# Optimization experiments

Measured on AMD Instinct MI355X. Metric: run time of the kernel, lower is better.

Reference implementation:

```python
import jax, jax.numpy as jnp
import numpy as np

B, S, H = 4, 4096, 1024
E, K, DE, DS = 8, 2, 128, 512  # n_routed_experts, top_k, routed hidden, shared hidden


def setup_inputs() -> dict:
    key = jax.random.key(0)
    ks = jax.random.split(key, 10)
    sc = 0.02
    return {
        "x": jax.random.normal(ks[0], (B, S, H), dtype=jnp.float32),
        "Wg": jax.random.normal(ks[1], (E, H), dtype=jnp.float32) * sc,
        "W1": jax.random.normal(ks[2], (E, DE, H), dtype=jnp.float32) * sc,
        "b1": jnp.zeros((E, DE), dtype=jnp.float32),
        "W2": jax.random.normal(ks[3], (E, H, DE), dtype=jnp.float32) * sc,
        "b2": jnp.zeros((E, H), dtype=jnp.float32),
        "Ws1": jax.random.normal(ks[4], (DS, H), dtype=jnp.float32) * sc,
        "bs1": jnp.zeros((DS,), dtype=jnp.float32),
        "Ws2": jax.random.normal(ks[5], (H, DS), dtype=jnp.float32) * sc,
        "bs2": jnp.zeros((H,), dtype=jnp.float32),
    }


def reference(x, Wg, W1, b1, W2, b2, Ws1, bs1, Ws2, bs2):
    # FFNMoE forward, eval mode (dropout = identity, aux loss inactive).
    xf = x.reshape(-1, H)  # [T, H]
    # --- MOEGate: softmax scoring + top-k + normalized weights ---
    logits = xf @ Wg.T                         # [T, E]
    scores = jax.nn.softmax(logits, axis=-1)
    topk_w, topk_idx = jax.lax.top_k(scores, K)  # [T, K]
    topk_w = topk_w / (jnp.sum(topk_w, axis=-1, keepdims=True) + 1e-20)
    # Dense per-(token, expert) combine weight (topk indices are distinct).
    w = jnp.sum(jax.nn.one_hot(topk_idx, E, dtype=xf.dtype) * topk_w[..., None], axis=1)  # [T, E]
    # --- Routed experts: fc1 -> relu -> fc2, weighted scatter-combine ---
    h1 = jax.nn.relu(jnp.einsum('th,efh->tef', xf, W1) + b1)       # [T, E, DE]
    y = jnp.einsum('tef,ehf,te->th', h1, W2, w) + w @ b2           # [T, H]
    # --- Shared expert ---
    sh = jax.nn.relu(xf @ Ws1.T + bs1) @ Ws2.T + bs2               # [T, H]
    return (y + sh).reshape(x.shape)
```

## Files before the change

kernel.cpp:

```cpp
#include <hip/hip_runtime.h>
#include <cstdint>

#define TTOK 16384
#define HD   1024
#define NE   8
#define NDE  128
#define NDS  512
#define NC1  1536
#define KC2  1536
#define NPAIR 28
#define MAXT  160
#define PREPB 3080
#define GATEB 1024
#define NH    768

typedef float  f32x4  __attribute__((ext_vector_type(4)));
typedef __bf16 bf16x8 __attribute__((ext_vector_type(8)));

__device__ __forceinline__ unsigned short f2bf(float f) {
  unsigned int u = __float_as_uint(f);
  u += 0x7fffu + ((u >> 16) & 1u);
  return (unsigned short)(u >> 16);
}

__device__ __forceinline__ void gl2lds16(const void* gp, void* lp) {
  void* g0 = const_cast<void*>(gp);
  __builtin_amdgcn_global_load_lds((__attribute__((address_space(1))) void*)g0,
                                   (__attribute__((address_space(3))) void*)lp,
                                   16, 0, 0);
}

__global__ __launch_bounds__(256) void prep_gate(
    const float* __restrict__ x, const float* __restrict__ Wg,
    const float* __restrict__ W1, const float* __restrict__ Ws1,
    const float* __restrict__ W2, const float* __restrict__ Ws2,
    const float* __restrict__ b1, const float* __restrict__ bs1,
    unsigned short* __restrict__ W1cat, unsigned short* __restrict__ W2cat,
    float* __restrict__ bias1, unsigned short* __restrict__ xbf,
    float2* __restrict__ wpair, int* __restrict__ pid) {
  if (blockIdx.x < PREPB) {
    const int total = NC1 * HD + HD * KC2 + NC1;
    for (int idx = blockIdx.x * 256 + threadIdx.x; idx < total; idx += PREPB * 256) {
      if (idx < NC1 * HD) {
        int r = idx >> 10, k = idx & 1023;
        float v = (r < 1024) ? W1[idx] : Ws1[(size_t)(r - 1024) * HD + k];
        W1cat[idx] = f2bf(v);
      } else if (idx < NC1 * HD + HD * KC2) {
        int i2 = idx - NC1 * HD;
        int h = i2 / KC2;
        int j = i2 - h * KC2;
        float v = (j < 1024) ? W2[(size_t)((j >> 7) * HD + h) * NDE + (j & 127)]
                             : Ws2[(size_t)h * NDS + (j - 1024)];
        W2cat[i2] = f2bf(v);
      } else {
        int r = idx - (NC1 * HD + HD * KC2);
        bias1[r] = (r < 1024) ? b1[r] : bs1[r - 1024];
      }
    }
    return;
  }
  __shared__ float part[16 * 8 * 64];
  __shared__ float lgs[128];

  const int tid  = threadIdx.x;
  const int lane = tid & 63;
  const int wv   = tid >> 6;
  const int g    = blockIdx.x - PREPB;
  const int tokb = g * 16 + wv * 4;

  const float* xr = x + (size_t)tokb * HD + lane * 16;
  float4 xv[4][4];
#pragma unroll
  for (int t = 0; t < 4; ++t)
#pragma unroll
    for (int c = 0; c < 4; ++c)
      xv[t][c] = ((const float4*)(xr + (size_t)t * HD))[c];

#pragma unroll
  for (int t = 0; t < 4; ++t) {
    unsigned short* xo = xbf + (size_t)(tokb + t) * HD + lane * 16;
    union { unsigned short us[8]; uint4 v; } pk;
    pk.us[0] = f2bf(xv[t][0].x); pk.us[1] = f2bf(xv[t][0].y);
    pk.us[2] = f2bf(xv[t][0].z); pk.us[3] = f2bf(xv[t][0].w);
    pk.us[4] = f2bf(xv[t][1].x); pk.us[5] = f2bf(xv[t][1].y);
    pk.us[6] = f2bf(xv[t][1].z); pk.us[7] = f2bf(xv[t][1].w);
    ((uint4*)xo)[0] = pk.v;
    pk.us[0] = f2bf(xv[t][2].x); pk.us[1] = f2bf(xv[t][2].y);
    pk.us[2] = f2bf(xv[t][2].z); pk.us[3] = f2bf(xv[t][2].w);
    pk.us[4] = f2bf(xv[t][3].x); pk.us[5] = f2bf(xv[t][3].y);
    pk.us[6] = f2bf(xv[t][3].z); pk.us[7] = f2bf(xv[t][3].w);
    ((uint4*)xo)[1] = pk.v;
  }

  float p[4][8];
#pragma unroll
  for (int t = 0; t < 4; ++t)
#pragma unroll
    for (int e = 0; e < 8; ++e) p[t][e] = 0.f;
#pragma unroll
  for (int e = 0; e < 8; ++e) {
    const float4* wr = (const float4*)(Wg + (size_t)e * HD + lane * 16);
    float4 w0 = wr[0], w1 = wr[1], w2 = wr[2], w3 = wr[3];
#pragma unroll
    for (int t = 0; t < 4; ++t) {
      p[t][e] = w0.x * xv[t][0].x + w0.y * xv[t][0].y + w0.z * xv[t][0].z + w0.w * xv[t][0].w +
                w1.x * xv[t][1].x + w1.y * xv[t][1].y + w1.z * xv[t][1].z + w1.w * xv[t][1].w +
                w2.x * xv[t][2].x + w2.y * xv[t][2].y + w2.z * xv[t][2].z + w2.w * xv[t][2].w +
                w3.x * xv[t][3].x + w3.y * xv[t][3].y + w3.z * xv[t][3].z + w3.w * xv[t][3].w;
    }
  }
#pragma unroll
  for (int t = 0; t < 4; ++t)
#pragma unroll
    for (int e = 0; e < 8; ++e) {
      int j = (wv * 4 + t) * 8 + e;
      part[j * 64 + ((lane + 4 * j) & 63)] = p[t][e];
    }
  __syncthreads();

  if (tid < 128) {
    float s = 0.f;
#pragma unroll
    for (int m = 0; m < 16; ++m) {
      int kk = (4 * m + 4 * tid) & 63;
      float4 v = *(const float4*)&part[tid * 64 + kk];
      s += v.x + v.y + v.z + v.w;
    }
    lgs[tid] = s;
  }
  __syncthreads();

  if (tid < 16) {
    float lg[8];
#pragma unroll
    for (int e = 0; e < 8; ++e) lg[e] = lgs[tid * 8 + e];
    int i1 = 0; float m1 = lg[0];
#pragma unroll
    for (int e = 1; e < 8; ++e) { if (lg[e] > m1) { m1 = lg[e]; i1 = e; } }
    int i2 = -1; float m2 = -3.4e38f;
#pragma unroll
    for (int e = 0; e < 8; ++e) { if (e != i1 && lg[e] > m2) { m2 = lg[e]; i2 = e; } }
    float Z = 0.f;
#pragma unroll
    for (int e = 0; e < 8; ++e) Z += expf(lg[e] - m1);
    float s1 = 1.f / Z;
    float s2 = expf(m2 - m1) / Z;
    float dn = s1 + s2 + 1e-20f;
    float w1 = s1 / dn, w2 = s2 / dn;
    int ef, es; float wf, wsx;
    if (i1 < i2) { ef = i1; es = i2; wf = w1; wsx = w2; }
    else         { ef = i2; es = i1; wf = w2; wsx = w1; }
    int pq = ef * 7 - (ef * (ef - 1)) / 2 + (es - ef - 1);
    int t = g * 16 + tid;
    wpair[t] = make_float2(wf, wsx);
    pid[t] = pq;
  }
}

__global__ __launch_bounds__(256) void route_scan(const int* __restrict__ pid,
                                                  int* __restrict__ perm,
                                                  int4* __restrict__ tiletab,
                                                  int* __restrict__ ntct) {
  __shared__ int hist[256 * 29];
  __shared__ int totals[NPAIR];
  __shared__ int spre[256];
  const int p   = blockIdx.x;
  const int tid = threadIdx.x;
#pragma unroll
  for (int q = 0; q < 29; ++q) hist[tid * 29 + q] = 0;
  __syncthreads();
  for (int k = 0; k < 64; ++k) {
    int q = pid[tid + (k << 8)];
    hist[tid * 29 + q]++;
  }
  __syncthreads();
  if (tid < NPAIR) {
    int s = 0;
    for (int i = 0; i < 256; ++i) s += hist[i * 29 + tid];
    totals[tid] = s;
  }
  __syncthreads();
  const int mycnt = hist[tid * 29 + p];
  spre[tid] = mycnt;
  __syncthreads();
  for (int d = 1; d < 256; d <<= 1) {
    int add = (tid >= d) ? spre[tid - d] : 0;
    __syncthreads();
    spre[tid] += add;
    __syncthreads();
  }
  int estart = 0, tstart = 0;
  for (int q = 0; q < p; ++q) { estart += totals[q]; tstart += (totals[q] + 127) >> 7; }
  const int cp = totals[p];
  const int nt = (cp + 127) >> 7;
  if (p == NPAIR - 1 && tid == 0) ntct[0] = tstart + nt;
  for (int k = tid; k < nt; k += 256) {
    int4 e;
    e.x = p;
    e.y = estart + (k << 7);
    e.z = min(128, cp - (k << 7));
    e.w = (tstart + k) << 7;
    tiletab[tstart + k] = e;
  }
  int wr = estart + spre[tid] - mycnt;
  for (int k = 0; k < 64; ++k) {
    int t = tid + (k << 8);
    if (pid[t] == p) perm[wr++] = t;
  }
}

__global__ __launch_bounds__(256) void moe_fc1(const unsigned short* __restrict__ xbf,
                                               const unsigned short* __restrict__ W1cat,
                                               const int* __restrict__ perm,
                                               const float2* __restrict__ wpair,
                                               const float* __restrict__ bias1,
                                               const int4* __restrict__ tiletab,
                                               const int* __restrict__ ntct,
                                               unsigned short* __restrict__ Hbuf) {
  const int L   = blockIdx.x;
  const int xcd = L & 7;
  const int s   = L >> 3;
  const int mg  = s / 6;
  const int nn  = s - mg * 6;
  const int mt  = xcd + (mg << 3);
  if (mt >= ntct[0]) return;
  const int4 tt = tiletab[mt];
  const int eoff = tt.y, valid = tt.z, hbase = tt.w;
  int ef = 0, rem = tt.x;
  while (rem >= 7 - ef) { rem -= 7 - ef; ef++; }
  const int es = ef + 1 + rem;
  const int brow = (nn == 0) ? ef * 128 : (nn == 1) ? es * 128 : 1024 + ((nn - 2) << 7);

  __shared__ __align__(16) unsigned short As[128 * 64];
  __shared__ __align__(16) unsigned short Bs[128 * 64];

  const int tid  = threadIdx.x;
  const int lane = tid & 63;
  const int wv   = tid >> 6;
  const int wm   = wv >> 1;
  const int wn   = wv & 1;
  const int r16  = lane & 15;
  const int quad = lane >> 4;

  const unsigned short* gA[4];
  const unsigned short* gB[4];
  unsigned short* lA[4];
  unsigned short* lB[4];
#pragma unroll
  for (int i = 0; i < 4; ++i) {
    int idx = i * 256 + tid;
    int row = idx >> 3;
    int cc  = idx & 7;
    int kc  = cc ^ (row & 7);
    int tok = perm[eoff + min(row, valid - 1)];
    gA[i] = xbf + (size_t)tok * HD + kc * 8;
    gB[i] = W1cat + (size_t)(brow + row) * HD + kc * 8;
    lA[i] = As + idx * 8;
    lB[i] = Bs + idx * 8;
  }

  int aoff[4], boff[4];
#pragma unroll
  for (int i = 0; i < 4; ++i) {
    int ra = wm * 64 + i * 16 + r16;
    aoff[i] = ra * 64 + ((quad ^ (ra & 7)) << 3);
    int rb = wn * 64 + i * 16 + r16;
    boff[i] = rb * 64 + ((quad ^ (rb & 7)) << 3);
  }

  f32x4 acc[4][4];
#pragma unroll
  for (int i = 0; i < 4; ++i)
#pragma unroll
    for (int j = 0; j < 4; ++j) acc[i][j] = (f32x4){0.f, 0.f, 0.f, 0.f};

  for (int kt = 0; kt < 16; ++kt) {
    const int ko = kt << 6;
#pragma unroll
    for (int i = 0; i < 4; ++i) gl2lds16(gA[i] + ko, lA[i]);
#pragma unroll
    for (int i = 0; i < 4; ++i) gl2lds16(gB[i] + ko, lB[i]);
    __syncthreads();
#pragma unroll
    for (int g = 0; g < 2; ++g) {
      const int gx = g << 5;
      bf16x8 av[4], bv[4];
#pragma unroll
      for (int i = 0; i < 4; ++i) av[i] = *(const bf16x8*)(As + (aoff[i] ^ gx));
#pragma unroll
      for (int j = 0; j < 4; ++j) bv[j] = *(const bf16x8*)(Bs + (boff[j] ^ gx));
#pragma unroll
      for (int i = 0; i < 4; ++i)
#pragma unroll
        for (int j = 0; j < 4; ++j)
          acc[i][j] = __builtin_amdgcn_mfma_f32_16x16x32_bf16(av[i], bv[j], acc[i][j], 0, 0, 0);
    }
    __syncthreads();
  }

  float* wl = (float*)As;
  if (tid < 128) {
    int tok = perm[eoff + min(tid, valid - 1)];
    float sc = 1.0f;
    if (nn == 0) sc = wpair[tok].x;
    else if (nn == 1) sc = wpair[tok].y;
    wl[tid] = sc;
  }
  __syncthreads();
#pragma unroll
  for (int j = 0; j < 4; ++j) {
    const int cin = wn * 64 + j * 16 + r16;
    const float bz = bias1[brow + cin];
#pragma unroll
    for (int i = 0; i < 4; ++i) {
#pragma unroll
      for (int r = 0; r < 4; ++r) {
        const int lrow = wm * 64 + i * 16 + quad * 4 + r;
        float v = fmaxf(acc[i][j][r] + bz, 0.f) * wl[lrow];
        Hbuf[(size_t)(hbase + lrow) * NH + nn * 128 + cin] = f2bf(v);
      }
    }
  }
}

__global__ __launch_bounds__(256) void moe_fc2(const unsigned short* __restrict__ Hbuf,
                                               const unsigned short* __restrict__ W2cat,
                                               const int* __restrict__ perm,
                                               const float2* __restrict__ wpair,
                                               const float* __restrict__ b2,
                                               const float* __restrict__ bs2,
                                               const int4* __restrict__ tiletab,
                                               const int* __restrict__ ntct,
                                               float* __restrict__ out) {
  const int L   = blockIdx.x;
  const int xcd = L & 7;
  const int s   = L >> 3;
  const int mg  = s >> 3;
  const int nn  = s & 7;
  const int mt  = xcd + (mg << 3);
  if (mt >= ntct[0]) return;
  const int4 tt = tiletab[mt];
  const int eoff = tt.y, valid = tt.z, hbase = tt.w;
  int ef = 0, rem = tt.x;
  while (rem >= 7 - ef) { rem -= 7 - ef; ef++; }
  const int es = ef + 1 + rem;
  const int tileN = nn << 7;

  __shared__ __align__(16) unsigned short As[128 * 64];
  __shared__ __align__(16) unsigned short Bs[128 * 64];

  const int tid  = threadIdx.x;
  const int lane = tid & 63;
  const int wv   = tid >> 6;
  const int wm   = wv >> 1;
  const int wn   = wv & 1;
  const int r16  = lane & 15;
  const int quad = lane >> 4;

  const unsigned short* gA[4];
  const unsigned short* gB[4];
  unsigned short* lA[4];
  unsigned short* lB[4];
#pragma unroll
  for (int i = 0; i < 4; ++i) {
    int idx = i * 256 + tid;
    int row = idx >> 3;
    int cc  = idx & 7;
    int kc  = cc ^ (row & 7);
    gA[i] = Hbuf + (size_t)(hbase + row) * NH + kc * 8;
    gB[i] = W2cat + (size_t)(tileN + row) * KC2 + kc * 8;
    lA[i] = As + idx * 8;
    lB[i] = Bs + idx * 8;
  }

  int aoff[4], boff[4];
#pragma unroll
  for (int i = 0; i < 4; ++i) {
    int ra = wm * 64 + i * 16 + r16;
    aoff[i] = ra * 64 + ((quad ^ (ra & 7)) << 3);
    int rb = wn * 64 + i * 16 + r16;
    boff[i] = rb * 64 + ((quad ^ (rb & 7)) << 3);
  }

  f32x4 acc[4][4];
#pragma unroll
  for (int i = 0; i < 4; ++i)
#pragma unroll
    for (int j = 0; j < 4; ++j) acc[i][j] = (f32x4){0.f, 0.f, 0.f, 0.f};

  for (int kt = 0; kt < 12; ++kt) {
    const int koA = kt << 6;
    const int koB = (kt < 2) ? ef * 128 + (kt << 6)
                 : (kt < 4) ? es * 128 + ((kt - 2) << 6)
                            : 1024 + ((kt - 4) << 6);
#pragma unroll
    for (int i = 0; i < 4; ++i) gl2lds16(gA[i] + koA, lA[i]);
#pragma unroll
    for (int i = 0; i < 4; ++i) gl2lds16(gB[i] + koB, lB[i]);
    __syncthreads();
#pragma unroll
    for (int g = 0; g < 2; ++g) {
      const int gx = g << 5;
      bf16x8 av[4], bv[4];
#pragma unroll
      for (int i = 0; i < 4; ++i) av[i] = *(const bf16x8*)(As + (aoff[i] ^ gx));
#pragma unroll
      for (int j = 0; j < 4; ++j) bv[j] = *(const bf16x8*)(Bs + (boff[j] ^ gx));
#pragma unroll
      for (int i = 0; i < 4; ++i)
#pragma unroll
        for (int j = 0; j < 4; ++j)
          acc[i][j] = __builtin_amdgcn_mfma_f32_16x16x32_bf16(av[i], bv[j], acc[i][j], 0, 0, 0);
    }
    __syncthreads();
  }

  float2* wl2 = (float2*)As;
  int* tokl   = (int*)Bs;
  if (tid < 128) {
    int tokc = perm[eoff + min(tid, valid - 1)];
    tokl[tid] = (tid < valid) ? tokc : -1;
    wl2[tid] = wpair[tokc];
  }
  __syncthreads();
  float bsc[4], b2a[4], b2b[4];
#pragma unroll
  for (int j = 0; j < 4; ++j) {
    const int col = tileN + wn * 64 + j * 16 + r16;
    bsc[j] = bs2[col];
    b2a[j] = b2[(size_t)ef * HD + col];
    b2b[j] = b2[(size_t)es * HD + col];
  }
#pragma unroll
  for (int i = 0; i < 4; ++i) {
#pragma unroll
    for (int r = 0; r < 4; ++r) {
      const int lrow = wm * 64 + i * 16 + quad * 4 + r;
      const int tok = tokl[lrow];
      if (tok < 0) continue;
      const float2 w = wl2[lrow];
#pragma unroll
      for (int j = 0; j < 4; ++j) {
        const int col = tileN + wn * 64 + j * 16 + r16;
        out[(size_t)tok * HD + col] = acc[i][j][r] + bsc[j] + w.x * b2a[j] + w.y * b2b[j];
      }
    }
  }
}

extern "C" void kernel_launch(void* const* d_in, const int* in_sizes, int n_in,
                              void* d_out, int out_size, void* d_ws, size_t ws_size,
                              hipStream_t stream) {
  const float* x   = (const float*)d_in[0];
  const float* Wg  = (const float*)d_in[1];
  const float* W1  = (const float*)d_in[2];
  const float* b1  = (const float*)d_in[3];
  const float* W2  = (const float*)d_in[4];
  const float* b2  = (const float*)d_in[5];
  const float* Ws1 = (const float*)d_in[6];
  const float* bs1 = (const float*)d_in[7];
  const float* Ws2 = (const float*)d_in[8];
  const float* bs2 = (const float*)d_in[9];

  char* ws = (char*)d_ws;
  size_t off = 0;
  unsigned short* xbf   = (unsigned short*)(ws + off); off += (size_t)TTOK * HD * 2;
  unsigned short* Hbuf  = (unsigned short*)(ws + off); off += (size_t)MAXT * 128 * NH * 2;
  unsigned short* W1cat = (unsigned short*)(ws + off); off += (size_t)NC1 * HD * 2;
  unsigned short* W2cat = (unsigned short*)(ws + off); off += (size_t)HD * KC2 * 2;
  float* bias1          = (float*)(ws + off);          off += (size_t)NC1 * 4;
  float2* wpair         = (float2*)(ws + off);         off += (size_t)TTOK * 8;
  int* pid              = (int*)(ws + off);            off += (size_t)TTOK * 4;
  int* perm             = (int*)(ws + off);            off += (size_t)TTOK * 4;
  int4* tiletab         = (int4*)(ws + off);           off += (size_t)MAXT * 16;
  int* ntct             = (int*)(ws + off);            off += 16;

  prep_gate<<<PREPB + GATEB, 256, 0, stream>>>(x, Wg, W1, Ws1, W2, Ws2, b1, bs1,
                                               W1cat, W2cat, bias1, xbf, wpair, pid);
  route_scan<<<NPAIR, 256, 0, stream>>>(pid, perm, tiletab, ntct);
  moe_fc1<<<8 * 20 * 6, 256, 0, stream>>>(xbf, W1cat, perm, wpair, bias1, tiletab, ntct, Hbuf);
  moe_fc2<<<8 * 20 * 8, 256, 0, stream>>>(Hbuf, W2cat, perm, wpair, b2, bs2, tiletab, ntct,
                                          (float*)d_out);
}
```

Measured before the change: 250.1 us.

## Use 256x256 tiles with double-buffered 8-wave pipelined MFMA GEMMs for MoE

```diff
diff --git a/kernel.cpp b/kernel.cpp
--- a/kernel.cpp
+++ b/kernel.cpp
@@ -9,7 +9,7 @@
 #define NC1  1536
 #define KC2  1536
 #define NPAIR 28
-#define MAXT  160
+#define MAXT  96
 #define PREPB 3080
 #define GATEB 1024
 #define NH    768
@@ -29,6 +29,60 @@
                                    (__attribute__((address_space(3))) void*)lp,
                                    16, 0, 0);
 }
+
+__device__ __forceinline__ void barx() {
+  asm volatile("" ::: "memory");
+  __builtin_amdgcn_s_barrier();
+  asm volatile("" ::: "memory");
+}
+
+template<int Q>
+__device__ __forceinline__ void phase_reads(const unsigned short* Ab, const unsigned short* Bb,
+                                            int bs, int a0, int b0,
+                                            bf16x8 (&av)[4][2], bf16x8 (&bv)[2][2]) {
+  constexpr int MH = Q >> 1, NHF = Q & 1;
+  if constexpr (NHF == 0) {
+#pragma unroll
+    for (int m = 0; m < 4; ++m) {
+      const int ao = a0 + (MH * 4 + m) * 1024;
+      av[m][0] = *(const bf16x8*)(Ab + bs + ao);
+      av[m][1] = *(const bf16x8*)(Ab + bs + (ao ^ 32));
+    }
+  }
+#pragma unroll
+  for (int n = 0; n < 2; ++n) {
+    const int bo = b0 + (NHF * 2 + n) * 1024;
+    bv[n][0] = *(const bf16x8*)(Bb + bs + bo);
+    bv[n][1] = *(const bf16x8*)(Bb + bs + (bo ^ 32));
+  }
+}
+
+template<int Q>
+__device__ __forceinline__ void phase_mfma(bf16x8 (&av)[4][2], bf16x8 (&bv)[2][2],
+                                           f32x4 (&acc)[8][4]) {
+  constexpr int MH = Q >> 1, NHF = Q & 1;
+  __builtin_amdgcn_s_setprio(1);
+#pragma unroll
+  for (int ks = 0; ks < 2; ++ks)
+#pragma unroll
+    for (int m = 0; m < 4; ++m)
+#pragma unroll
+      for (int n = 0; n < 2; ++n)
+        acc[MH * 4 + m][NHF * 2 + n] = __builtin_amdgcn_mfma_f32_16x16x32_bf16(
+            av[m][ks], bv[n][ks], acc[MH * 4 + m][NHF * 2 + n], 0, 0, 0);
+  __builtin_amdgcn_s_setprio(0);
+}
+
+#define PH(Q, BH, STG, VMW) do {                                    \
+    phase_reads<Q>(AsB, BsB, (BH) * 16384, a0, b0, av, bv);         \
+    STG;                                                            \
+    VMW;                                                            \
+    barx();                                                         \
+    asm volatile("s_waitcnt lgkmcnt(0)" ::: "memory");              \
+    __builtin_amdgcn_sched_barrier(0);                              \
+    phase_mfma<Q>(av, bv, acc);                                     \
+    barx();                                                         \
+  } while (0)
 
 __global__ __launch_bounds__(256) void prep_gate(
     const float* __restrict__ x, const float* __restrict__ Wg,
@@ -190,16 +244,16 @@
     __syncthreads();
   }
   int estart = 0, tstart = 0;
-  for (int q = 0; q < p; ++q) { estart += totals[q]; tstart += (totals[q] + 127) >> 7; }
+  for (int q = 0; q < p; ++q) { estart += totals[q]; tstart += (totals[q] + 255) >> 8; }
   const int cp = totals[p];
-  const int nt = (cp + 127) >> 7;
+  const int nt = (cp + 255) >> 8;
   if (p == NPAIR - 1 && tid == 0) ntct[0] = tstart + nt;
   for (int k = tid; k < nt; k += 256) {
     int4 e;
     e.x = p;
-    e.y = estart + (k << 7);
-    e.z = min(128, cp - (k << 7));
-    e.w = (tstart + k) << 7;
+    e.y = estart + (k << 8);
+    e.z = min(256, cp - (k << 8));
+    e.w = (tstart + k) << 8;
     tiletab[tstart + k] = e;
   }
   int wr = estart + spre[tid] - mycnt;
@@ -209,19 +263,16 @@
   }
 }
 
-__global__ __launch_bounds__(256) void moe_fc1(const unsigned short* __restrict__ xbf,
-                                               const unsigned short* __restrict__ W1cat,
-                                               const int* __restrict__ perm,
-                                               const float2* __restrict__ wpair,
-                                               const float* __restrict__ bias1,
-                                               const int4* __restrict__ tiletab,
-                                               const int* __restrict__ ntct,
-                                               unsigned short* __restrict__ Hbuf) {
+__global__ __launch_bounds__(512, 2) void moe_fc1(
+    const unsigned short* __restrict__ xbf, const unsigned short* __restrict__ W1cat,
+    const int* __restrict__ perm, const float2* __restrict__ wpair,
+    const float* __restrict__ bias1, const int4* __restrict__ tiletab,
+    const int* __restrict__ ntct, unsigned short* __restrict__ Hbuf) {
   const int L   = blockIdx.x;
   const int xcd = L & 7;
   const int s   = L >> 3;
-  const int mg  = s / 6;
-  const int nn  = s - mg * 6;
+  const int mg  = s / 3;
+  const int nn  = s - mg * 3;
   const int mt  = xcd + (mg << 3);
   if (mt >= ntct[0]) return;
   const int4 tt = tiletab[mt];
@@ -229,114 +280,138 @@
   int ef = 0, rem = tt.x;
   while (rem >= 7 - ef) { rem -= 7 - ef; ef++; }
   const int es = ef + 1 + rem;
-  const int brow = (nn == 0) ? ef * 128 : (nn == 1) ? es * 128 : 1024 + ((nn - 2) << 7);
-
-  __shared__ __align__(16) unsigned short As[128 * 64];
-  __shared__ __align__(16) unsigned short Bs[128 * 64];
+
+  __shared__ __align__(16) unsigned short As[2 * 16384];
+  __shared__ __align__(16) unsigned short Bs[2 * 16384];
 
   const int tid  = threadIdx.x;
   const int lane = tid & 63;
   const int wv   = tid >> 6;
-  const int wm   = wv >> 1;
-  const int wn   = wv & 1;
+  const int wm   = wv >> 2;
+  const int wn   = wv & 3;
   const int r16  = lane & 15;
   const int quad = lane >> 4;
 
-  const unsigned short* gA[4];
-  const unsigned short* gB[4];
-  unsigned short* lA[4];
-  unsigned short* lB[4];
-#pragma unroll
-  for (int i = 0; i < 4; ++i) {
-    int idx = i * 256 + tid;
-    int row = idx >> 3;
-    int cc  = idx & 7;
-    int kc  = cc ^ (row & 7);
-    int tok = perm[eoff + min(row, valid - 1)];
-    gA[i] = xbf + (size_t)tok * HD + kc * 8;
-    gB[i] = W1cat + (size_t)(brow + row) * HD + kc * 8;
-    lA[i] = As + idx * 8;
-    lB[i] = Bs + idx * 8;
-  }
-
-  int aoff[4], boff[4];
-#pragma unroll
-  for (int i = 0; i < 4; ++i) {
-    int ra = wm * 64 + i * 16 + r16;
-    aoff[i] = ra * 64 + ((quad ^ (ra & 7)) << 3);
-    int rb = wn * 64 + i * 16 + r16;
-    boff[i] = rb * 64 + ((quad ^ (rb & 7)) << 3);
-  }
-
-  f32x4 acc[4][4];
-#pragma unroll
-  for (int i = 0; i < 4; ++i)
+  const unsigned short* gAp[2][2];
+  const unsigned short* gBp[2][2];
+  int lAo[2][2], lBo[2][2];
+#pragma unroll
+  for (int h = 0; h < 2; ++h)
+#pragma unroll
+    for (int jj = 0; jj < 2; ++jj) {
+      const int id = jj * 512 + tid;
+      const int rp = id >> 3, cc = id & 7;
+      const int rowA = h * 64 + ((rp & 64) << 1) + (rp & 63);
+      const int tok  = perm[eoff + min(rowA, valid - 1)];
+      gAp[h][jj] = xbf + (size_t)tok * HD + ((cc ^ (rowA & 7)) << 3);
+      lAo[h][jj] = rowA * 64 + cc * 8;
+      const int rowB = h * 128 + rp;
+      const int brow = (nn == 0) ? (((h == 0) ? ef : es) * 128 + rp)
+                                 : 1024 + (nn - 1) * 256 + rowB;
+      gBp[h][jj] = W1cat + (size_t)brow * HD + ((cc ^ (rowB & 7)) << 3);
+      lBo[h][jj] = rowB * 64 + cc * 8;
+    }
+
+  unsigned short* AsB = As;
+  unsigned short* BsB = Bs;
+
+  const int swz = (quad ^ (r16 & 7)) << 3;
+  const int a0 = (wm * 128 + r16) * 64 + swz;
+  const int b0 = (wn * 64 + r16) * 64 + swz;
+
+  f32x4 acc[8][4];
+#pragma unroll
+  for (int i = 0; i < 8; ++i)
 #pragma unroll
     for (int j = 0; j < 4; ++j) acc[i][j] = (f32x4){0.f, 0.f, 0.f, 0.f};
-
-  for (int kt = 0; kt < 16; ++kt) {
-    const int ko = kt << 6;
-#pragma unroll
-    for (int i = 0; i < 4; ++i) gl2lds16(gA[i] + ko, lA[i]);
-#pragma unroll
-    for (int i = 0; i < 4; ++i) gl2lds16(gB[i] + ko, lB[i]);
-    __syncthreads();
-#pragma unroll
-    for (int g = 0; g < 2; ++g) {
-      const int gx = g << 5;
-      bf16x8 av[4], bv[4];
-#pragma unroll
-      for (int i = 0; i < 4; ++i) av[i] = *(const bf16x8*)(As + (aoff[i] ^ gx));
-#pragma unroll
-      for (int j = 0; j < 4; ++j) bv[j] = *(const bf16x8*)(Bs + (boff[j] ^ gx));
-#pragma unroll
-      for (int i = 0; i < 4; ++i)
-#pragma unroll
-        for (int j = 0; j < 4; ++j)
-          acc[i][j] = __builtin_amdgcn_mfma_f32_16x16x32_bf16(av[i], bv[j], acc[i][j], 0, 0, 0);
-    }
-    __syncthreads();
-  }
-
-  float* wl = (float*)As;
-  if (tid < 128) {
-    int tok = perm[eoff + min(tid, valid - 1)];
-    float sc = 1.0f;
-    if (nn == 0) sc = wpair[tok].x;
-    else if (nn == 1) sc = wpair[tok].y;
-    wl[tid] = sc;
-  }
-  __syncthreads();
-#pragma unroll
-  for (int j = 0; j < 4; ++j) {
-    const int cin = wn * 64 + j * 16 + r16;
-    const float bz = bias1[brow + cin];
-#pragma unroll
-    for (int i = 0; i < 4; ++i) {
-#pragma unroll
-      for (int r = 0; r < 4; ++r) {
-        const int lrow = wm * 64 + i * 16 + quad * 4 + r;
-        float v = fmaxf(acc[i][j][r] + bz, 0.f) * wl[lrow];
-        Hbuf[(size_t)(hbase + lrow) * NH + nn * 128 + cin] = f2bf(v);
+  bf16x8 av[4][2], bv[2][2];
+
+#define STG_A1K(t, h) do { const int b_ = (((t) & 1) << 14); const int o_ = ((t) << 6); \
+    gl2lds16(gAp[h][0] + o_, AsB + b_ + lAo[h][0]);                                     \
+    gl2lds16(gAp[h][1] + o_, AsB + b_ + lAo[h][1]); } while (0)
+#define STG_B1K(t, h) do { const int b_ = (((t) & 1) << 14); const int o_ = ((t) << 6); \
+    gl2lds16(gBp[h][0] + o_, BsB + b_ + lBo[h][0]);                                     \
+    gl2lds16(gBp[h][1] + o_, BsB + b_ + lBo[h][1]); } while (0)
+
+  STG_A1K(0, 0); STG_A1K(0, 1);
+  STG_B1K(0, 0); STG_B1K(0, 1);
+  STG_A1K(1, 0); STG_A1K(1, 1);
+  asm volatile("s_waitcnt vmcnt(4)" ::: "memory");
+  barx();
+
+#define FC1_ITER(it, LASTF) do {                                                   \
+    const int O1 = 2 * (it) + 1, E2 = 2 * (it) + 2, O2 = 2 * (it) + 3;             \
+    PH(0, 0, STG_B1K(O1, 0), (void)0);                                             \
+    PH(1, 0, STG_B1K(O1, 1), (void)0);                                             \
+    PH(2, 0, { if (!(LASTF)) STG_A1K(E2, 0); }, (void)0);                          \
+    PH(3, 0, { if (!(LASTF)) STG_A1K(E2, 1); },                                    \
+        { if (LASTF) asm volatile("s_waitcnt vmcnt(0)" ::: "memory");              \
+          else       asm volatile("s_waitcnt vmcnt(4)" ::: "memory"); });          \
+    PH(0, 1, { if (!(LASTF)) STG_B1K(E2, 0); }, (void)0);                          \
+    PH(1, 1, { if (!(LASTF)) STG_B1K(E2, 1); }, (void)0);                          \
+    PH(2, 1, { if (!(LASTF)) STG_A1K(O2, 0); }, (void)0);                          \
+    PH(3, 1, { if (!(LASTF)) STG_A1K(O2, 1); },                                    \
+        { if (LASTF) asm volatile("s_waitcnt vmcnt(0)" ::: "memory");              \
+          else       asm volatile("s_waitcnt vmcnt(4)" ::: "memory"); });          \
+  } while (0)
+
+#pragma unroll 1
+  for (int it = 0; it < 7; ++it) FC1_ITER(it, 0);
+  FC1_ITER(7, 1);
+
+  __syncthreads();
+  float2* wl = (float2*)As;
+  if (tid < 256) {
+    const int tokc = perm[eoff + min(tid, valid - 1)];
+    wl[tid] = wpair[tokc];
+  }
+  __syncthreads();
+  float bz[4];
+  const int colb = wn * 64 + r16;
+#pragma unroll
+  for (int n2 = 0; n2 < 4; ++n2) {
+    const int col = colb + n2 * 16;
+    const int bidx = (nn == 0) ? ((col < 128) ? ef * 128 + col : es * 128 + (col - 128))
+                               : 1024 + (nn - 1) * 256 + col;
+    bz[n2] = bias1[bidx];
+  }
+#pragma unroll
+  for (int m2 = 0; m2 < 8; ++m2) {
+#pragma unroll
+    for (int r = 0; r < 4; ++r) {
+      const int lrow = wm * 128 + m2 * 16 + quad * 4 + r;
+      const float2 w = wl[lrow];
+      const float sc = (nn == 0) ? ((wn < 2) ? w.x : w.y) : 1.0f;
+      unsigned short* hp = Hbuf + (size_t)(hbase + lrow) * NH + nn * 256 + colb;
+#pragma unroll
+      for (int n2 = 0; n2 < 4; ++n2) {
+        const float v = fmaxf(acc[m2][n2][r] + bz[n2], 0.f) * sc;
+        hp[n2 * 16] = f2bf(v);
       }
     }
   }
-}
-
-__global__ __launch_bounds__(256) void moe_fc2(const unsigned short* __restrict__ Hbuf,
-                                               const unsigned short* __restrict__ W2cat,
-                                               const int* __restrict__ perm,
-                                               const float2* __restrict__ wpair,
-                                               const float* __restrict__ b2,
-                                               const float* __restrict__ bs2,
-                                               const int4* __restrict__ tiletab,
-                                               const int* __restrict__ ntct,
-                                               float* __restrict__ out) {
+#undef FC1_ITER
+#undef STG_A1K
+#undef STG_B1K
+}
+
+__device__ __forceinline__ int koB2(int t, int ef, int es) {
+  return (t < 2) ? ef * 128 + (t << 6)
+       : (t < 4) ? es * 128 + ((t - 2) << 6)
+                 : 1024 + ((t - 4) << 6);
+}
+
+__global__ __launch_bounds__(512, 2) void moe_fc2(
+    const unsigned short* __restrict__ Hbuf, const unsigned short* __restrict__ W2cat,
+    const int* __restrict__ perm, const float2* __restrict__ wpair,
+    const float* __restrict__ b2, const float* __restrict__ bs2,
+    const int4* __restrict__ tiletab, const int* __restrict__ ntct,
+    float* __restrict__ out) {
   const int L   = blockIdx.x;
   const int xcd = L & 7;
   const int s   = L >> 3;
-  const int mg  = s >> 3;
-  const int nn  = s & 7;
+  const int mg  = s >> 2;
+  const int nn  = s & 3;
   const int mt  = xcd + (mg << 3);
   if (mt >= ntct[0]) return;
   const int4 tt = tiletab[mt];
@@ -344,108 +419,118 @@
   int ef = 0, rem = tt.x;
   while (rem >= 7 - ef) { rem -= 7 - ef; ef++; }
   const int es = ef + 1 + rem;
-  const int tileN = nn << 7;
-
-  __shared__ __align__(16) unsigned short As[128 * 64];
-  __shared__ __align__(16) unsigned short Bs[128 * 64];
+  const int tileN = nn << 8;
+
+  __shared__ __align__(16) unsigned short As[2 * 16384];
+  __shared__ __align__(16) unsigned short Bs[2 * 16384];
 
   const int tid  = threadIdx.x;
   const int lane = tid & 63;
   const int wv   = tid >> 6;
-  const int wm   = wv >> 1;
-  const int wn   = wv & 1;
+  const int wm   = wv >> 2;
+  const int wn   = wv & 3;
   const int r16  = lane & 15;
   const int quad = lane >> 4;
 
-  const unsigned short* gA[4];
-  const unsigned short* gB[4];
-  unsigned short* lA[4];
-  unsigned short* lB[4];
-#pragma unroll
-  for (int i = 0; i < 4; ++i) {
-    int idx = i * 256 + tid;
-    int row = idx >> 3;
-    int cc  = idx & 7;
-    int kc  = cc ^ (row & 7);
-    gA[i] = Hbuf + (size_t)(hbase + row) * NH + kc * 8;
-    gB[i] = W2cat + (size_t)(tileN + row) * KC2 + kc * 8;
-    lA[i] = As + idx * 8;
-    lB[i] = Bs + idx * 8;
-  }
-
-  int aoff[4], boff[4];
-#pragma unroll
-  for (int i = 0; i < 4; ++i) {
-    int ra = wm * 64 + i * 16 + r16;
-    aoff[i] = ra * 64 + ((quad ^ (ra & 7)) << 3);
-    int rb = wn * 64 + i * 16 + r16;
-    boff[i] = rb * 64 + ((quad ^ (rb & 7)) << 3);
-  }
-
-  f32x4 acc[4][4];
-#pragma unroll
-  for (int i = 0; i < 4; ++i)
+  const unsigned short* gAp[2][2];
+  const unsigned short* gBp[2][2];
+  int lAo[2][2], lBo[2][2];
+#pragma unroll
+  for (int h = 0; h < 2; ++h)
+#pragma unroll
+    for (int jj = 0; jj < 2; ++jj) {
+      const int id = jj * 512 + tid;
+      const int rp = id >> 3, cc = id & 7;
+      const int rowA = h * 64 + ((rp & 64) << 1) + (rp & 63);
+      gAp[h][jj] = Hbuf + (size_t)(hbase + rowA) * NH + ((cc ^ (rowA & 7)) << 3);
+      lAo[h][jj] = rowA * 64 + cc * 8;
+      const int rowB = h * 128 + rp;
+      gBp[h][jj] = W2cat + (size_t)(tileN + rowB) * KC2 + ((cc ^ (rowB & 7)) << 3);
+      lBo[h][jj] = rowB * 64 + cc * 8;
+    }
+
+  unsigned short* AsB = As;
+  unsigned short* BsB = Bs;
+
+  const int swz = (quad ^ (r16 & 7)) << 3;
+  const int a0 = (wm * 128 + r16) * 64 + swz;
+  const int b0 = (wn * 64 + r16) * 64 + swz;
+
+  f32x4 acc[8][4];
+#pragma unroll
+  for (int i = 0; i < 8; ++i)
 #pragma unroll
     for (int j = 0; j < 4; ++j) acc[i][j] = (f32x4){0.f, 0.f, 0.f, 0.f};
-
-  for (int kt = 0; kt < 12; ++kt) {
-    const int koA = kt << 6;
-    const int koB = (kt < 2) ? ef * 128 + (kt << 6)
-                 : (kt < 4) ? es * 128 + ((kt - 2) << 6)
-                            : 1024 + ((kt - 4) << 6);
-#pragma unroll
-    for (int i = 0; i < 4; ++i) gl2lds16(gA[i] + koA, lA[i]);
-#pragma unroll
-    for (int i = 0; i < 4; ++i) gl2lds16(gB[i] + koB, lB[i]);
-    __syncthreads();
-#pragma unroll
-    for (int g = 0; g < 2; ++g) {
-      const int gx = g << 5;
-      bf16x8 av[4], bv[4];
-#pragma unroll
-      for (int i = 0; i < 4; ++i) av[i] = *(const bf16x8*)(As + (aoff[i] ^ gx));
-#pragma unroll
-      for (int j = 0; j < 4; ++j) bv[j] = *(const bf16x8*)(Bs + (boff[j] ^ gx));
-#pragma unroll
-      for (int i = 0; i < 4; ++i)
-#pragma unroll
-        for (int j = 0; j < 4; ++j)
-          acc[i][j] = __builtin_amdgcn_mfma_f32_16x16x32_bf16(av[i], bv[j], acc[i][j], 0, 0, 0);
-    }
-    __syncthreads();
-  }
-
+  bf16x8 av[4][2], bv[2][2];
+
+#define STG_A2K(t, h) do { const int b_ = (((t) & 1) << 14); const int o_ = ((t) << 6); \
+    gl2lds16(gAp[h][0] + o_, AsB + b_ + lAo[h][0]);                                     \
+    gl2lds16(gAp[h][1] + o_, AsB + b_ + lAo[h][1]); } while (0)
+#define STG_B2K(t, h) do { const int b_ = (((t) & 1) << 14); const int o_ = koB2((t), ef, es); \
+    gl2lds16(gBp[h][0] + o_, BsB + b_ + lBo[h][0]);                                     \
+    gl2lds16(gBp[h][1] + o_, BsB + b_ + lBo[h][1]); } while (0)
+
+  STG_A2K(0, 0); STG_A2K(0, 1);
+  STG_B2K(0, 0); STG_B2K(0, 1);
+  STG_A2K(1, 0); STG_A2K(1, 1);
+  asm volatile("s_waitcnt vmcnt(4)" ::: "memory");
+  barx();
+
+#define FC2_ITER(it, LASTF) do {                                                   \
+    const int O1 = 2 * (it) + 1, E2 = 2 * (it) + 2, O2 = 2 * (it) + 3;             \
+    PH(0, 0, STG_B2K(O1, 0), (void)0);                                             \
+    PH(1, 0, STG_B2K(O1, 1), (void)0);                                             \
+    PH(2, 0, { if (!(LASTF)) STG_A2K(E2, 0); }, (void)0);                          \
+    PH(3, 0, { if (!(LASTF)) STG_A2K(E2, 1); },                                    \
+        { if (LASTF) asm volatile("s_waitcnt vmcnt(0)" ::: "memory");              \
+          else       asm volatile("s_waitcnt vmcnt(4)" ::: "memory"); });          \
+    PH(0, 1, { if (!(LASTF)) STG_B2K(E2, 0); }, (void)0);                          \
+    PH(1, 1, { if (!(LASTF)) STG_B2K(E2, 1); }, (void)0);                          \
+    PH(2, 1, { if (!(LASTF)) STG_A2K(O2, 0); }, (void)0);                          \
+    PH(3, 1, { if (!(LASTF)) STG_A2K(O2, 1); },                                    \
+        { if (LASTF) asm volatile("s_waitcnt vmcnt(0)" ::: "memory");              \
+          else       asm volatile("s_waitcnt vmcnt(4)" ::: "memory"); });          \
+  } while (0)
+
+#pragma unroll 1
+  for (int it = 0; it < 5; ++it) FC2_ITER(it, 0);
+  FC2_ITER(5, 1);
+
+  __syncthreads();
   float2* wl2 = (float2*)As;
   int* tokl   = (int*)Bs;
-  if (tid < 128) {
-    int tokc = perm[eoff + min(tid, valid - 1)];
+  if (tid < 256) {
+    const int tokc = perm[eoff + min(tid, valid - 1)];
     tokl[tid] = (tid < valid) ? tokc : -1;
     wl2[tid] = wpair[tokc];
   }
   __syncthreads();
   float bsc[4], b2a[4], b2b[4];
-#pragma unroll
-  for (int j = 0; j < 4; ++j) {
-    const int col = tileN + wn * 64 + j * 16 + r16;
-    bsc[j] = bs2[col];
-    b2a[j] = b2[(size_t)ef * HD + col];
-    b2b[j] = b2[(size_t)es * HD + col];
-  }
-#pragma unroll
-  for (int i = 0; i < 4; ++i) {
+  const int colb = tileN + wn * 64 + r16;
+#pragma unroll
+  for (int n2 = 0; n2 < 4; ++n2) {
+    const int col = colb + n2 * 16;
+    bsc[n2] = bs2[col];
+    b2a[n2] = b2[(size_t)ef * HD + col];
+    b2b[n2] = b2[(size_t)es * HD + col];
+  }
+#pragma unroll
+  for (int m2 = 0; m2 < 8; ++m2) {
 #pragma unroll
     for (int r = 0; r < 4; ++r) {
-      const int lrow = wm * 64 + i * 16 + quad * 4 + r;
+      const int lrow = wm * 128 + m2 * 16 + quad * 4 + r;
       const int tok = tokl[lrow];
       if (tok < 0) continue;
       const float2 w = wl2[lrow];
-#pragma unroll
-      for (int j = 0; j < 4; ++j) {
-        const int col = tileN + wn * 64 + j * 16 + r16;
-        out[(size_t)tok * HD + col] = acc[i][j][r] + bsc[j] + w.x * b2a[j] + w.y * b2b[j];
-      }
-    }
-  }
+      float* op = out + (size_t)tok * HD + colb;
+#pragma unroll
+      for (int n2 = 0; n2 < 4; ++n2)
+        op[n2 * 16] = acc[m2][n2][r] + bsc[n2] + w.x * b2a[n2] + w.y * b2b[n2];
+    }
+  }
+#undef FC2_ITER
+#undef STG_A2K
+#undef STG_B2K
 }
 
 extern "C" void kernel_launch(void* const* d_in, const int* in_sizes, int n_in,
@@ -465,7 +550,7 @@
   char* ws = (char*)d_ws;
   size_t off = 0;
   unsigned short* xbf   = (unsigned short*)(ws + off); off += (size_t)TTOK * HD * 2;
-  unsigned short* Hbuf  = (unsigned short*)(ws + off); off += (size_t)MAXT * 128 * NH * 2;
+  unsigned short* Hbuf  = (unsigned short*)(ws + off); off += (size_t)MAXT * 256 * NH * 2;
   unsigned short* W1cat = (unsigned short*)(ws + off); off += (size_t)NC1 * HD * 2;
   unsigned short* W2cat = (unsigned short*)(ws + off); off += (size_t)HD * KC2 * 2;
   float* bias1          = (float*)(ws + off);          off += (size_t)NC1 * 4;
@@ -478,7 +563,7 @@
   prep_gate<<<PREPB + GATEB, 256, 0, stream>>>(x, Wg, W1, Ws1, W2, Ws2, b1, bs1,
                                                W1cat, W2cat, bias1, xbf, wpair, pid);
   route_scan<<<NPAIR, 256, 0, stream>>>(pid, perm, tiletab, ntct);
-  moe_fc1<<<8 * 20 * 6, 256, 0, stream>>>(xbf, W1cat, perm, wpair, bias1, tiletab, ntct, Hbuf);
-  moe_fc2<<<8 * 20 * 8, 256, 0, stream>>>(Hbuf, W2cat, perm, wpair, b2, bs2, tiletab, ntct,
+  moe_fc1<<<8 * 12 * 3, 512, 0, stream>>>(xbf, W1cat, perm, wpair, bias1, tiletab, ntct, Hbuf);
+  moe_fc2<<<8 * 12 * 4, 512, 0, stream>>>(Hbuf, W2cat, perm, wpair, b2, bs2, tiletab, ntct,
                                           (float*)d_out);
 }
```

After: 294.7 us. +17.8%, slower.

## Double-buffer LDS tiles in both MoE GEMM kernels with async prefetch

Applied to the files above, without the earlier changes.

```diff
diff --git a/kernel.cpp b/kernel.cpp
--- a/kernel.cpp
+++ b/kernel.cpp
@@ -29,6 +29,14 @@
                                    (__attribute__((address_space(3))) void*)lp,
                                    16, 0, 0);
 }
+
+__device__ __forceinline__ void barx() {
+  asm volatile("" ::: "memory");
+  __builtin_amdgcn_s_barrier();
+  asm volatile("" ::: "memory");
+}
+#define VM8  asm volatile("s_waitcnt vmcnt(8)" ::: "memory")
+#define VM0  asm volatile("s_waitcnt vmcnt(0)" ::: "memory")
 
 __global__ __launch_bounds__(256) void prep_gate(
     const float* __restrict__ x, const float* __restrict__ Wg,
@@ -231,8 +239,8 @@
   const int es = ef + 1 + rem;
   const int brow = (nn == 0) ? ef * 128 : (nn == 1) ? es * 128 : 1024 + ((nn - 2) << 7);
 
-  __shared__ __align__(16) unsigned short As[128 * 64];
-  __shared__ __align__(16) unsigned short Bs[128 * 64];
+  __shared__ __align__(16) unsigned short As[2 * 128 * 64];
+  __shared__ __align__(16) unsigned short Bs[2 * 128 * 64];
 
   const int tid  = threadIdx.x;
   const int lane = tid & 63;
@@ -274,30 +282,44 @@
 #pragma unroll
     for (int j = 0; j < 4; ++j) acc[i][j] = (f32x4){0.f, 0.f, 0.f, 0.f};
 
-  for (int kt = 0; kt < 16; ++kt) {
-    const int ko = kt << 6;
-#pragma unroll
-    for (int i = 0; i < 4; ++i) gl2lds16(gA[i] + ko, lA[i]);
-#pragma unroll
-    for (int i = 0; i < 4; ++i) gl2lds16(gB[i] + ko, lB[i]);
-    __syncthreads();
-#pragma unroll
-    for (int g = 0; g < 2; ++g) {
-      const int gx = g << 5;
-      bf16x8 av[4], bv[4];
-#pragma unroll
-      for (int i = 0; i < 4; ++i) av[i] = *(const bf16x8*)(As + (aoff[i] ^ gx));
-#pragma unroll
-      for (int j = 0; j < 4; ++j) bv[j] = *(const bf16x8*)(Bs + (boff[j] ^ gx));
-#pragma unroll
-      for (int i = 0; i < 4; ++i)
-#pragma unroll
-        for (int j = 0; j < 4; ++j)
-          acc[i][j] = __builtin_amdgcn_mfma_f32_16x16x32_bf16(av[i], bv[j], acc[i][j], 0, 0, 0);
-    }
-    __syncthreads();
-  }
-
+#define STAGE1(kt, b) do { const int ko_ = (kt) << 6; const int lo_ = (b) * 8192;        \
+    _Pragma("unroll")                                                                    \
+    for (int i_ = 0; i_ < 4; ++i_) gl2lds16(gA[i_] + ko_, lA[i_] + lo_);                 \
+    _Pragma("unroll")                                                                    \
+    for (int i_ = 0; i_ < 4; ++i_) gl2lds16(gB[i_] + ko_, lB[i_] + lo_); } while (0)
+
+#define COMP1(b) do { const int lo_ = (b) * 8192;                                        \
+    _Pragma("unroll")                                                                    \
+    for (int g_ = 0; g_ < 2; ++g_) {                                                     \
+      const int gx_ = g_ << 5;                                                           \
+      bf16x8 av_[4], bv_[4];                                                             \
+      _Pragma("unroll")                                                                  \
+      for (int i_ = 0; i_ < 4; ++i_) av_[i_] = *(const bf16x8*)(As + lo_ + (aoff[i_] ^ gx_)); \
+      _Pragma("unroll")                                                                  \
+      for (int j_ = 0; j_ < 4; ++j_) bv_[j_] = *(const bf16x8*)(Bs + lo_ + (boff[j_] ^ gx_)); \
+      _Pragma("unroll")                                                                  \
+      for (int i_ = 0; i_ < 4; ++i_)                                                     \
+        _Pragma("unroll")                                                                \
+        for (int j_ = 0; j_ < 4; ++j_)                                                   \
+          acc[i_][j_] = __builtin_amdgcn_mfma_f32_16x16x32_bf16(av_[i_], bv_[j_], acc[i_][j_], 0, 0, 0); \
+    } } while (0)
+
+  STAGE1(0, 0);
+#pragma unroll 1
+  for (int kt = 0; kt < 16; kt += 2) {
+    if (kt + 1 < 16) { STAGE1(kt + 1, 1); VM8; } else { VM0; }
+    barx();
+    COMP1(0);
+    barx();
+    if (kt + 2 < 16) { STAGE1(kt + 2, 0); VM8; } else { VM0; }
+    barx();
+    COMP1(1);
+    barx();
+  }
+#undef STAGE1
+#undef COMP1
+
+  __syncthreads();
   float* wl = (float*)As;
   if (tid < 128) {
     int tok = perm[eoff + min(tid, valid - 1)];
@@ -346,8 +368,8 @@
   const int es = ef + 1 + rem;
   const int tileN = nn << 7;
 
-  __shared__ __align__(16) unsigned short As[128 * 64];
-  __shared__ __align__(16) unsigned short Bs[128 * 64];
+  __shared__ __align__(16) unsigned short As[2 * 128 * 64];
+  __shared__ __align__(16) unsigned short Bs[2 * 128 * 64];
 
   const int tid  = threadIdx.x;
   const int lane = tid & 63;
@@ -388,33 +410,49 @@
 #pragma unroll
     for (int j = 0; j < 4; ++j) acc[i][j] = (f32x4){0.f, 0.f, 0.f, 0.f};
 
-  for (int kt = 0; kt < 12; ++kt) {
-    const int koA = kt << 6;
-    const int koB = (kt < 2) ? ef * 128 + (kt << 6)
-                 : (kt < 4) ? es * 128 + ((kt - 2) << 6)
-                            : 1024 + ((kt - 4) << 6);
-#pragma unroll
-    for (int i = 0; i < 4; ++i) gl2lds16(gA[i] + koA, lA[i]);
-#pragma unroll
-    for (int i = 0; i < 4; ++i) gl2lds16(gB[i] + koB, lB[i]);
-    __syncthreads();
-#pragma unroll
-    for (int g = 0; g < 2; ++g) {
-      const int gx = g << 5;
-      bf16x8 av[4], bv[4];
-#pragma unroll
-      for (int i = 0; i < 4; ++i) av[i] = *(const bf16x8*)(As + (aoff[i] ^ gx));
-#pragma unroll
-      for (int j = 0; j < 4; ++j) bv[j] = *(const bf16x8*)(Bs + (boff[j] ^ gx));
-#pragma unroll
-      for (int i = 0; i < 4; ++i)
-#pragma unroll
-        for (int j = 0; j < 4; ++j)
-          acc[i][j] = __builtin_amdgcn_mfma_f32_16x16x32_bf16(av[i], bv[j], acc[i][j], 0, 0, 0);
-    }
-    __syncthreads();
-  }
-
+#define KOB2(kt) ((kt) < 2 ? ef * 128 + ((kt) << 6)                       \
+                : (kt) < 4 ? es * 128 + (((kt) - 2) << 6)                 \
+                           : 1024 + (((kt) - 4) << 6))
+#define STAGE2(kt, b) do { const int koA_ = (kt) << 6; const int koB_ = KOB2(kt);        \
+    const int lo_ = (b) * 8192;                                                          \
+    _Pragma("unroll")                                                                    \
+    for (int i_ = 0; i_ < 4; ++i_) gl2lds16(gA[i_] + koA_, lA[i_] + lo_);                \
+    _Pragma("unroll")                                                                    \
+    for (int i_ = 0; i_ < 4; ++i_) gl2lds16(gB[i_] + koB_, lB[i_] + lo_); } while (0)
+
+#define COMP2(b) do { const int lo_ = (b) * 8192;                                        \
+    _Pragma("unroll")                                                                    \
+    for (int g_ = 0; g_ < 2; ++g_) {                                                     \
+      const int gx_ = g_ << 5;                                                           \
+      bf16x8 av_[4], bv_[4];                                                             \
+      _Pragma("unroll")                                                                  \
+      for (int i_ = 0; i_ < 4; ++i_) av_[i_] = *(const bf16x8*)(As + lo_ + (aoff[i_] ^ gx_)); \
+      _Pragma("unroll")                                                                  \
+      for (int j_ = 0; j_ < 4; ++j_) bv_[j_] = *(const bf16x8*)(Bs + lo_ + (boff[j_] ^ gx_)); \
+      _Pragma("unroll")                                                                  \
+      for (int i_ = 0; i_ < 4; ++i_)                                                     \
+        _Pragma("unroll")                                                                \
+        for (int j_ = 0; j_ < 4; ++j_)                                                   \
+          acc[i_][j_] = __builtin_amdgcn_mfma_f32_16x16x32_bf16(av_[i_], bv_[j_], acc[i_][j_], 0, 0, 0); \
+    } } while (0)
+
+  STAGE2(0, 0);
+#pragma unroll 1
+  for (int kt = 0; kt < 12; kt += 2) {
+    if (kt + 1 < 12) { STAGE2(kt + 1, 1); VM8; } else { VM0; }
+    barx();
+    COMP2(0);
+    barx();
+    if (kt + 2 < 12) { STAGE2(kt + 2, 0); VM8; } else { VM0; }
+    barx();
+    COMP2(1);
+    barx();
+  }
+#undef STAGE2
+#undef COMP2
+#undef KOB2
+
+  __syncthreads();
   float2* wl2 = (float2*)As;
   int* tokl   = (int*)Bs;
   if (tid < 128) {
```

Result: no change. 253.0 us (+1.1%).
